# Optimization experiments

Hardware: AMD Instinct MI355X
Metric: run time of the kernel (lower is better)

The kernel has to match this reference:

```python
import jax, jax.numpy as jnp
import numpy as np


def setup_inputs() -> dict:
    key = jax.random.key(0)
    ks = jax.random.split(key, 8)
    B, S, D, H, E = 4, 2048, 1024, 2048, 8
    s = 0.02  # init scale
    return {
        "x": jax.random.normal(ks[0], (B, S, D), dtype=jnp.float32),
        "gate_w": jax.random.normal(ks[1], (E, D), dtype=jnp.float32) * s,
        "w1": jax.random.normal(ks[2], (E, H, D), dtype=jnp.float32) * s,
        "b1": jnp.zeros((E, H), dtype=jnp.float32),
        "w2": jax.random.normal(ks[3], (E, H, D), dtype=jnp.float32) * s,
        "b2": jnp.zeros((E, H), dtype=jnp.float32),
        "w3": jax.random.normal(ks[4], (E, D, H), dtype=jnp.float32) * s,
        "b3": jnp.zeros((E, D), dtype=jnp.float32),
        "topk": 2,
    }


def reference(x, gate_w, w1, b1, w2, b2, w3, b3, topk):
    D = x.shape[-1]
    E = gate_w.shape[0]
    xf = x.reshape(-1, D)                      # [T, D]
    T = xf.shape[0]

    logits = xf @ gate_w.T                     # [T, E]
    vals, idx = jax.lax.top_k(logits, topk)    # [T, K]
    wts = jax.nn.softmax(vals, axis=-1)        # [T, K]

    # per-token combine weight per expert (0 if expert not in top-k)
    comb = jnp.zeros((T, E), dtype=xf.dtype).at[
        jnp.arange(T)[:, None], idx
    ].add(wts)                                 # [T, E]

    out = jnp.zeros_like(xf)
    for e in range(E):  # fixed small loop over experts
        h = (xf @ w1[e].T + b1[e]) * jax.nn.silu(xf @ w2[e].T + b2[e])  # [T, H]
        y = h @ w3[e].T + b3[e]                                           # [T, D]
        out = out + comb[:, e:e + 1] * y
    return out.reshape(x.shape)
```

## Files before the change

### kernel.cpp

```cpp
#include <hip/hip_runtime.h>
#include <hip/hip_bf16.h>
#include <stdint.h>

#define T_TOK   8192
#define D_DIM   1024
#define H_DIM   2048
#define E_EXP   8
#define NP2     4096
#define BM      256
#define CAP     (2*T_TOK + E_EXP*BM)
#define MAXMB   (CAP/BM)

using f32x4 = __attribute__((ext_vector_type(4))) float;
using s16x4 = __attribute__((ext_vector_type(4))) short;
using s16x8 = __attribute__((ext_vector_type(8))) short;

__device__ __forceinline__ short bf16_of(float f) {
  union { float f; unsigned u; } v; v.f = f;
  unsigned r = v.u + 0x7FFFu + ((v.u >> 16) & 1u);
  return (short)(r >> 16);
}
__device__ __forceinline__ float f_of_bf16(short s) {
  union { unsigned u; float f; } v; v.u = ((unsigned)(unsigned short)s) << 16;
  return v.f;
}

__device__ __forceinline__ void gload16(const void* g, void* l) {
  __builtin_amdgcn_global_load_lds(
      (const __attribute__((address_space(1))) unsigned int*)g,
      (__attribute__((address_space(3))) unsigned int*)l, 16, 0, 0);
}

__global__ __launch_bounds__(256) void conv_w12(const float* __restrict__ w1,
                                                const float* __restrict__ w2,
                                                short* __restrict__ w12b) {
  int idx = blockIdx.x * 256 + threadIdx.x;
  int e = idx >> 20;
  int rem = idx & 0xFFFFF;
  int np = rem >> 8;
  int kc = rem & 255;
  int g = np >> 5, tt = np & 31, half = tt >> 4, srow = g * 16 + (tt & 15);
  const f32x4* src = (const f32x4*)(half ? w2 : w1) + ((size_t)e * H_DIM + srow) * 256 + kc;
  f32x4 v = *src;
  s16x4 o;
  o[0] = bf16_of(v[0]); o[1] = bf16_of(v[1]); o[2] = bf16_of(v[2]); o[3] = bf16_of(v[3]);
  ((s16x4*)w12b)[idx] = o;
}

__global__ __launch_bounds__(256) void conv_w3(const float* __restrict__ w3,
                                               short* __restrict__ w3b) {
  int idx = blockIdx.x * 256 + threadIdx.x;
  f32x4 v = ((const f32x4*)w3)[idx];
  s16x4 o;
  o[0] = bf16_of(v[0]); o[1] = bf16_of(v[1]); o[2] = bf16_of(v[2]); o[3] = bf16_of(v[3]);
  ((s16x4*)w3b)[idx] = o;
}

__global__ __launch_bounds__(256) void gate_kernel(const float* __restrict__ x,
                                                   const float* __restrict__ gw,
                                                   int* __restrict__ tok_e,
                                                   float* __restrict__ gatew) {
  __shared__ float g[E_EXP * D_DIM];
  int tid = threadIdx.x;
  for (int i = tid; i < E_EXP * 256; i += 256)
    ((f32x4*)g)[i] = ((const f32x4*)gw)[i];
  __syncthreads();
  int w = tid >> 6, lane = tid & 63;
  int t = blockIdx.x * 4 + w;
  float acc[E_EXP] = {};
  const f32x4* xrow = (const f32x4*)(x + (size_t)t * D_DIM);
#pragma unroll
  for (int i = 0; i < 4; ++i) {
    f32x4 xv = xrow[lane + 64 * i];
#pragma unroll
    for (int e = 0; e < E_EXP; ++e) {
      f32x4 gv = ((const f32x4*)g)[e * 256 + lane + 64 * i];
      acc[e] += xv[0] * gv[0] + xv[1] * gv[1] + xv[2] * gv[2] + xv[3] * gv[3];
    }
  }
#pragma unroll
  for (int e = 0; e < E_EXP; ++e)
#pragma unroll
    for (int off = 1; off < 64; off <<= 1)
      acc[e] += __shfl_xor(acc[e], off);
  if (lane == 0) {
    int i0 = 0; float v0 = acc[0];
    for (int e = 1; e < E_EXP; ++e) if (acc[e] > v0) { v0 = acc[e]; i0 = e; }
    int i1 = -1; float v1 = -1e30f;
    for (int e = 0; e < E_EXP; ++e) if (e != i0 && acc[e] > v1) { v1 = acc[e]; i1 = e; }
    float z = __expf(v1 - v0);
    tok_e[2 * t] = i0; tok_e[2 * t + 1] = i1;
    gatew[2 * t] = 1.f / (1.f + z); gatew[2 * t + 1] = z / (1.f + z);
  }
}

__global__ __launch_bounds__(256) void hist_kernel(const int* __restrict__ tok_e,
                                                   int* __restrict__ counts) {
  __shared__ int bc[E_EXP];
  const int tid = threadIdx.x, lane = tid & 63;
  if (tid < E_EXP) bc[tid] = 0;
  __syncthreads();
  const int4 v = ((const int4*)tok_e)[blockIdx.x * 256 + tid];
#pragma unroll
  for (int e = 0; e < E_EXP; ++e) {
    int cnt = __popcll(__ballot(v.x == e)) + __popcll(__ballot(v.y == e)) +
              __popcll(__ballot(v.z == e)) + __popcll(__ballot(v.w == e));
    if (lane == 0 && cnt) atomicAdd(&bc[e], cnt);
  }
  __syncthreads();
  if (tid < E_EXP && bc[tid]) atomicAdd(&counts[tid], bc[tid]);
}

__global__ void scan_kernel(const int* __restrict__ counts, int* __restrict__ off,
                            int* __restrict__ mb2e, int* __restrict__ mb2row) {
  if (threadIdx.x == 0 && blockIdx.x == 0) {
    int acc = 0, mb = 0;
    for (int e = 0; e < E_EXP; ++e) {
      off[e] = acc;
      int nb = (counts[e] + BM - 1) / BM;
      for (int b = 0; b < nb; ++b) { mb2e[mb] = e; mb2row[mb] = acc + b * BM; ++mb; }
      acc += nb * BM;
    }
    off[E_EXP] = acc;
    for (; mb < MAXMB; ++mb) mb2e[mb] = -1;
  }
}

__global__ __launch_bounds__(256) void assign_kernel(const int* __restrict__ tok_e,
                                                     const int* __restrict__ off,
                                                     int* __restrict__ fill,
                                                     int* __restrict__ perm,
                                                     int* __restrict__ tok_slot) {
  __shared__ int wcnt[4][E_EXP];
  __shared__ int wbase[4][E_EXP];
  const int tid = threadIdx.x, lane = tid & 63, wid = tid >> 6;
  if (tid < 32) wcnt[tid >> 3][tid & 7] = 0;
  __syncthreads();
  const int ent = blockIdx.x * 256 + tid;
  const int e = tok_e[ent];
  int myrank = 0;
#pragma unroll
  for (int e0 = 0; e0 < E_EXP; ++e0) {
    unsigned long long m = __ballot(e == e0);
    if (e == e0) {
      myrank = __popcll(m & ((1ull << lane) - 1ull));
      if (myrank == 0) wcnt[wid][e0] = __popcll(m);
    }
  }
  __syncthreads();
  if (tid < E_EXP) {
    int tot = wcnt[0][tid] + wcnt[1][tid] + wcnt[2][tid] + wcnt[3][tid];
    int base = tot ? atomicAdd(&fill[tid], tot) : 0;
#pragma unroll
    for (int w = 0; w < 4; ++w) { wbase[w][tid] = base; base += wcnt[w][tid]; }
  }
  __syncthreads();
  const int slot = off[e] + wbase[wid][e] + myrank;
  perm[slot] = ent >> 1;
  tok_slot[ent] = slot;
}

__global__ __launch_bounds__(128) void gather_kernel(const float* __restrict__ x,
                                                     const int* __restrict__ off,
                                                     const int* __restrict__ counts,
                                                     const int* __restrict__ perm,
                                                     short* __restrict__ Xp) {
  int s = blockIdx.x, tid = threadIdx.x;
  int e = -1;
#pragma unroll
  for (int i = 0; i < E_EXP; ++i)
    if (s >= off[i] && s < off[i + 1]) { e = i; break; }
  bool valid = false; int t = 0;
  if (e >= 0) { int r = s - off[e]; if (r < counts[e]) { valid = true; t = perm[s]; } }
  s16x8 o;
  if (valid) {
    const f32x4* xr = (const f32x4*)(x + (size_t)t * D_DIM);
    f32x4 a = xr[tid * 2], b = xr[tid * 2 + 1];
    o[0] = bf16_of(a[0]); o[1] = bf16_of(a[1]); o[2] = bf16_of(a[2]); o[3] = bf16_of(a[3]);
    o[4] = bf16_of(b[0]); o[5] = bf16_of(b[1]); o[6] = bf16_of(b[2]); o[7] = bf16_of(b[3]);
  } else {
#pragma unroll
    for (int j = 0; j < 8; ++j) o[j] = 0;
  }
  *(s16x8*)(Xp + (size_t)s * D_DIM + tid * 8) = o;
}

template <int K, int BN_, int EPI>
__global__ __launch_bounds__(512, (BN_ == 128) ? 4 : 2)
void gemm256(const short* __restrict__ A,
             const short* __restrict__ Bw,
             const int* __restrict__ mb2e,
             const int* __restrict__ mb2row,
             const float* __restrict__ biasA,
             const float* __restrict__ biasB,
             short* __restrict__ Out) {
  constexpr int NFULL = (EPI == 0) ? NP2 : D_DIM;
  constexpr int OUTLD = (EPI == 0) ? H_DIM : D_DIM;
  constexpr int KB = K * 2;
  constexpr int NT = K / 32;
  constexpr int NBF = BN_ / 64;
  constexpr int ABYTES = 16384;
  constexpr int BBYTES = BN_ * 64;
  constexpr int BUFB = ABYTES + BBYTES;
  constexpr int NB_LOADS = BN_ / 128;

  const int mb = blockIdx.y;
  const int e = mb2e[mb];
  if (e < 0) return;
  const int row0 = mb2row[mb];
  const int bn = blockIdx.x;

  __shared__ alignas(16) char lds[3 * BUFB];

  const int tid = threadIdx.x;
  const int lane = tid & 63;
  const int wid = tid >> 6;
  const int wr = wid >> 2;
  const int wc = wid & 3;

  const char* gA = (const char*)(A + (size_t)row0 * K);
  const char* gB = (const char*)(Bw + ((size_t)e * NFULL + (size_t)bn * BN_) * K);

  const int srow0 = tid >> 2, spq = tid & 3;

  f32x4 acc[8][NBF] = {};

  auto stageA = [&](int kt, int buf) {
#pragma unroll
    for (int r = 0; r < 2; ++r) {
      const int row = r * 128 + srow0;
      const int lq = spq ^ ((row >> 1) & 3);
      gload16(gA + (size_t)row * KB + kt * 64 + lq * 16,
              lds + buf * BUFB + r * 8192 + tid * 16);
    }
  };
  auto stageB = [&](int kt, int buf) {
#pragma unroll
    for (int r = 0; r < NB_LOADS; ++r) {
      const int row = r * 128 + srow0;
      const int lq = spq ^ ((row >> 1) & 3);
      gload16(gB + (size_t)row * KB + kt * 64 + lq * 16,
              lds + buf * BUFB + ABYTES + r * 8192 + tid * 16);
    }
  };

  stageA(0, 0); stageB(0, 0);
  stageA(1, 1); stageB(1, 1);
  if constexpr (BN_ == 256) asm volatile("s_waitcnt vmcnt(4)" ::: "memory");
  else                      asm volatile("s_waitcnt vmcnt(3)" ::: "memory");
  __builtin_amdgcn_s_barrier();
  __builtin_amdgcn_sched_barrier(0);

  const int qsw = (((lane >> 4) ^ ((lane >> 1) & 3)) << 4);
  const int arow = wr * 128 + (lane & 15);
  const int brow = wc * (BN_ / 4) + (lane & 15);

  int bc = 0;
  int b2 = 2;
  for (int t = 0; t < NT; ++t) {
    const char* bufb = lds + bc * BUFB;
    const char* pa = bufb + arow * 64 + qsw;
    const char* pb = bufb + ABYTES + brow * 64 + qsw;
    s16x8 av[4], bv[NBF];
#pragma unroll
    for (int f = 0; f < NBF; ++f) bv[f] = *(const s16x8*)(pb + f * 1024);
#pragma unroll
    for (int f = 0; f < 4; ++f) av[f] = *(const s16x8*)(pa + f * 1024);
    if (t + 2 < NT) stageA(t + 2, b2);
    __builtin_amdgcn_s_barrier();
    asm volatile("s_waitcnt lgkmcnt(0)" ::: "memory");
    __builtin_amdgcn_sched_barrier(0);
    __builtin_amdgcn_s_setprio(1);
#pragma unroll
    for (int mf = 0; mf < 4; ++mf)
#pragma unroll
      for (int nf = 0; nf < NBF; ++nf)
        acc[mf][nf] = __builtin_amdgcn_mfma_f32_16x16x32_bf16(av[mf], bv[nf], acc[mf][nf], 0, 0, 0);
    __builtin_amdgcn_s_setprio(0);
    __builtin_amdgcn_sched_barrier(0);
    __builtin_amdgcn_s_barrier();
#pragma unroll
    for (int f = 0; f < 4; ++f) av[f] = *(const s16x8*)(pa + (4 + f) * 1024);
    if (t + 2 < NT) stageB(t + 2, b2);
    __builtin_amdgcn_s_barrier();
    asm volatile("s_waitcnt lgkmcnt(0)" ::: "memory");
    __builtin_amdgcn_sched_barrier(0);
    __builtin_amdgcn_s_setprio(1);
#pragma unroll
    for (int mf = 0; mf < 4; ++mf)
#pragma unroll
      for (int nf = 0; nf < NBF; ++nf)
        acc[4 + mf][nf] = __builtin_amdgcn_mfma_f32_16x16x32_bf16(av[mf], bv[nf], acc[4 + mf][nf], 0, 0, 0);
    __builtin_amdgcn_s_setprio(0);
    __builtin_amdgcn_sched_barrier(0);
    if (t < NT - 1) {
      if (t == NT - 2)          asm volatile("s_waitcnt vmcnt(0)" ::: "memory");
      else if (BN_ == 256)      asm volatile("s_waitcnt vmcnt(4)" ::: "memory");
      else                      asm volatile("s_waitcnt vmcnt(3)" ::: "memory");
      __builtin_amdgcn_s_barrier();
      __builtin_amdgcn_sched_barrier(0);
    }
    bc = (bc == 2) ? 0 : bc + 1;
    b2 = (b2 == 2) ? 0 : b2 + 1;
  }

  if constexpr (EPI == 0) {
#pragma unroll
    for (int mf = 0; mf < 8; ++mf) {
      const int mrow = row0 + wr * 128 + mf * 16 + ((lane >> 4) << 2);
#pragma unroll
      for (int p = 0; p < 2; ++p) {
        const int hcol = bn * 128 + wc * 32 + p * 16 + (lane & 15);
        const float bb1 = biasA[e * H_DIM + hcol];
        const float bb2 = biasB[e * H_DIM + hcol];
        const f32x4 a1 = acc[mf][2 * p], a2 = acc[mf][2 * p + 1];
#pragma unroll
        for (int j = 0; j < 4; ++j) {
          float x1 = a1[j] + bb1, x2 = a2[j] + bb2;
          float hv = x1 * (x2 / (1.f + __expf(-x2)));
          Out[(size_t)(mrow + j) * OUTLD + hcol] = bf16_of(hv);
        }
      }
    }
  } else {
#pragma unroll
    for (int mf = 0; mf < 8; ++mf) {
      const int mrow = row0 + wr * 128 + mf * 16 + ((lane >> 4) << 2);
#pragma unroll
      for (int nf = 0; nf < NBF; ++nf) {
        const int col = bn * BN_ + wc * (BN_ / 4) + nf * 16 + (lane & 15);
        const float bb = biasA[e * D_DIM + col];
#pragma unroll
        for (int j = 0; j < 4; ++j)
          Out[(size_t)(mrow + j) * OUTLD + col] = bf16_of(acc[mf][nf][j] + bb);
      }
    }
  }
}

__global__ __launch_bounds__(128) void combine_kernel(const short* __restrict__ ysb,
                                                      const int* __restrict__ tok_slot,
                                                      const float* __restrict__ gatew,
                                                      float* __restrict__ out) {
  int t = blockIdx.x, tid = threadIdx.x;
  int s0 = tok_slot[2 * t], s1 = tok_slot[2 * t + 1];
  float w0 = gatew[2 * t], w1 = gatew[2 * t + 1];
  s16x8 a = *(const s16x8*)(ysb + (size_t)s0 * D_DIM + tid * 8);
  s16x8 b = *(const s16x8*)(ysb + (size_t)s1 * D_DIM + tid * 8);
  float* op = out + (size_t)t * D_DIM + tid * 8;
  f32x4 o0, o1;
#pragma unroll
  for (int j = 0; j < 4; ++j) o0[j] = w0 * f_of_bf16(a[j]) + w1 * f_of_bf16(b[j]);
#pragma unroll
  for (int j = 0; j < 4; ++j) o1[j] = w0 * f_of_bf16(a[4 + j]) + w1 * f_of_bf16(b[4 + j]);
  *(f32x4*)op = o0;
  *(f32x4*)(op + 4) = o1;
}

extern "C" void kernel_launch(void* const* d_in, const int* in_sizes, int n_in,
                              void* d_out, int out_size, void* d_ws, size_t ws_size,
                              hipStream_t stream) {
  const float* x  = (const float*)d_in[0];
  const float* gw = (const float*)d_in[1];
  const float* w1 = (const float*)d_in[2];
  const float* b1 = (const float*)d_in[3];
  const float* w2 = (const float*)d_in[4];
  const float* b2 = (const float*)d_in[5];
  const float* w3 = (const float*)d_in[6];
  const float* b3 = (const float*)d_in[7];
  float* out = (float*)d_out;

  char* ws = (char*)d_ws;
  size_t o = 0;
  short* w12b = (short*)(ws + o); o += (size_t)E_EXP * NP2 * D_DIM * 2;
  short* w3b  = (short*)(ws + o); o += (size_t)E_EXP * D_DIM * H_DIM * 2;
  short* Xp   = (short*)(ws + o); o += (size_t)CAP * D_DIM * 2;
  short* ysb  = Xp;
  short* hbuf = (short*)(ws + o); o += (size_t)CAP * H_DIM * 2;
  int* meta     = (int*)(ws + o);
  int* counts   = meta;
  int* fill     = meta + 8;
  int* offv     = meta + 16;
  int* mb2e     = meta + 32;
  int* mb2row   = meta + 112;
  int* tok_e    = meta + 192;
  int* tok_slot = tok_e + 2 * T_TOK;
  int* perm     = tok_slot + 2 * T_TOK;
  float* gatew  = (float*)(perm + CAP);
  const size_t ws_needed = o + (192 + 4 * T_TOK + CAP + 2 * T_TOK) * sizeof(int);
  if (ws_size < ws_needed) return;

  hipMemsetAsync(counts, 0, 16 * sizeof(int), stream);

  conv_w12<<<(E_EXP * NP2 * 256) / 256, 256, 0, stream>>>(w1, w2, w12b);
  conv_w3 <<<(E_EXP * D_DIM * (H_DIM / 4)) / 256, 256, 0, stream>>>(w3, w3b);
  gate_kernel<<<T_TOK / 4, 256, 0, stream>>>(x, gw, tok_e, gatew);
  hist_kernel<<<(2 * T_TOK) / 1024, 256, 0, stream>>>(tok_e, counts);
  scan_kernel<<<1, 64, 0, stream>>>(counts, offv, mb2e, mb2row);
  assign_kernel<<<(2 * T_TOK) / 256, 256, 0, stream>>>(tok_e, offv, fill, perm, tok_slot);
  gather_kernel<<<CAP, 128, 0, stream>>>(x, offv, counts, perm, Xp);
  gemm256<D_DIM, 256, 0><<<dim3(NP2 / 256, MAXMB), 512, 0, stream>>>(Xp, w12b, mb2e, mb2row, b1, b2, hbuf);
  gemm256<H_DIM, 128, 1><<<dim3(D_DIM / 128, MAXMB), 512, 0, stream>>>(hbuf, w3b, mb2e, mb2row, b3, b3, ysb);
  combine_kernel<<<T_TOK, 128, 0, stream>>>(ysb, tok_slot, gatew, out);
}
```

Before: 408.5 us.

## Add double-buffered K64 gate/up GEMM, trim barriers, widen down-proj tile

Replaces the first expert GEMM with a new kernel that stages 64-wide K slices into two 64KB LDS buffers and interleaves the next slice's global loads with four MFMA phases. In the generic GEMM it removes the intra-iteration barriers and lgkmcnt waits between the two MFMA halves. The down-projection is switched to a 256-wide N tile, which halves its grid columns. Dropping the barriers relies on the existing vmcnt/barrier at the end of each iteration to keep LDS reuse safe. The 128KB LDS kernel and the wider tile may lower occupancy.

```diff
diff --git a/kernel.cpp b/kernel.cpp
--- a/kernel.cpp
+++ b/kernel.cpp
@@ -183,6 +183,121 @@
     for (int j = 0; j < 8; ++j) o[j] = 0;
   }
   *(s16x8*)(Xp + (size_t)s * D_DIM + tid * 8) = o;
+}
+
+__global__ __launch_bounds__(512, 2)
+void gemm12_k64(const short* __restrict__ A,
+                const short* __restrict__ Bw,
+                const int* __restrict__ mb2e,
+                const int* __restrict__ mb2row,
+                const float* __restrict__ b1v,
+                const float* __restrict__ b2v,
+                short* __restrict__ Out) {
+  constexpr int K = D_DIM;
+  constexpr int NT = K / 64;
+  constexpr int BUFB = 65536;
+  __shared__ alignas(16) char lds[2 * BUFB];
+
+  const int mb = blockIdx.y;
+  const int e = mb2e[mb];
+  if (e < 0) return;
+  const int row0 = mb2row[mb];
+  const int bn = blockIdx.x;
+
+  const int tid = threadIdx.x;
+  const int lane = tid & 63;
+  const int wid = tid >> 6;
+  const int wr = wid >> 2, wc = wid & 3;
+
+  const char* gA = (const char*)(A + (size_t)row0 * K);
+  const char* gB = (const char*)(Bw + ((size_t)e * NP2 + (size_t)bn * 256) * K);
+
+  auto stage_unit = [&](const char* g, int kt, int ks, char* dst) {
+#pragma unroll
+    for (int r = 0; r < 2; ++r) {
+      const int row = r * 128 + (tid >> 2);
+      const int lq = (tid & 3) ^ ((row >> 1) & 3);
+      gload16(g + (size_t)row * (K * 2) + kt * 128 + ks * 64 + lq * 16,
+              dst + r * 8192 + tid * 16);
+    }
+  };
+
+  f32x4 acc[8][4] = {};
+
+  stage_unit(gB, 0, 0, lds + 32768);
+  stage_unit(gA, 0, 0, lds + 0);
+  stage_unit(gB, 0, 1, lds + 49152);
+  stage_unit(gA, 0, 1, lds + 16384);
+  asm volatile("s_waitcnt vmcnt(4)" ::: "memory");
+  __builtin_amdgcn_s_barrier();
+  __builtin_amdgcn_sched_barrier(0);
+
+  const int qsw = (((lane >> 4) ^ ((lane >> 1) & 3)) << 4);
+  const int arow = wr * 128 + (lane & 15);
+  const int brow = wc * 64 + (lane & 15);
+
+  for (int t = 0; t < NT; ++t) {
+    char* cur = lds + (t & 1) * BUFB;
+    char* nxt = lds + ((t + 1) & 1) * BUFB;
+    const bool more = (t + 1 < NT);
+    s16x8 bv[4];
+#pragma unroll
+    for (int p = 0; p < 4; ++p) {
+      const int ks = p >> 1, half = p & 1;
+      const char* abase = cur + ks * 16384;
+      s16x8 av[4];
+      if (half == 0) {
+        const char* bbase = cur + 32768 + ks * 16384;
+#pragma unroll
+        for (int f = 0; f < 4; ++f)
+          bv[f] = *(const s16x8*)(bbase + (size_t)(brow + f * 16) * 64 + qsw);
+      }
+#pragma unroll
+      for (int f = 0; f < 4; ++f)
+        av[f] = *(const s16x8*)(abase + (size_t)(arow + half * 64 + f * 16) * 64 + qsw);
+      if (more) {
+        if (p == 0)      stage_unit(gB, t + 1, 0, nxt + 32768);
+        else if (p == 1) stage_unit(gA, t + 1, 0, nxt + 0);
+        else if (p == 2) stage_unit(gB, t + 1, 1, nxt + 49152);
+        else             stage_unit(gA, t + 1, 1, nxt + 16384);
+      }
+      if (p == 1) {
+        if (t == NT - 1) asm volatile("s_waitcnt vmcnt(0)" ::: "memory");
+        else             asm volatile("s_waitcnt vmcnt(4)" ::: "memory");
+      }
+      if (p == 3 && t < NT - 1) asm volatile("s_waitcnt vmcnt(4)" ::: "memory");
+      __builtin_amdgcn_s_barrier();
+      asm volatile("s_waitcnt lgkmcnt(0)" ::: "memory");
+      __builtin_amdgcn_sched_barrier(0);
+      __builtin_amdgcn_s_setprio(1);
+#pragma unroll
+      for (int mf2 = 0; mf2 < 4; ++mf2)
+#pragma unroll
+        for (int nf = 0; nf < 4; ++nf)
+          acc[half * 4 + mf2][nf] =
+              __builtin_amdgcn_mfma_f32_16x16x32_bf16(av[mf2], bv[nf], acc[half * 4 + mf2][nf], 0, 0, 0);
+      __builtin_amdgcn_s_setprio(0);
+      __builtin_amdgcn_s_barrier();
+    }
+  }
+
+#pragma unroll
+  for (int mf = 0; mf < 8; ++mf) {
+    const int mrow = row0 + wr * 128 + (mf >> 2) * 64 + (mf & 3) * 16 + ((lane >> 4) << 2);
+#pragma unroll
+    for (int p = 0; p < 2; ++p) {
+      const int hcol = bn * 128 + wc * 32 + p * 16 + (lane & 15);
+      const float bb1 = b1v[e * H_DIM + hcol];
+      const float bb2 = b2v[e * H_DIM + hcol];
+      const f32x4 a1 = acc[mf][2 * p], a2 = acc[mf][2 * p + 1];
+#pragma unroll
+      for (int j = 0; j < 4; ++j) {
+        float x1 = a1[j] + bb1, x2 = a2[j] + bb2;
+        float hv = x1 * (x2 / (1.f + __expf(-x2)));
+        Out[(size_t)(mrow + j) * H_DIM + hcol] = bf16_of(hv);
+      }
+    }
+  }
 }
 
 template <int K, int BN_, int EPI>
@@ -267,9 +382,6 @@
 #pragma unroll
     for (int f = 0; f < 4; ++f) av[f] = *(const s16x8*)(pa + f * 1024);
     if (t + 2 < NT) stageA(t + 2, b2);
-    __builtin_amdgcn_s_barrier();
-    asm volatile("s_waitcnt lgkmcnt(0)" ::: "memory");
-    __builtin_amdgcn_sched_barrier(0);
     __builtin_amdgcn_s_setprio(1);
 #pragma unroll
     for (int mf = 0; mf < 4; ++mf)
@@ -277,14 +389,9 @@
       for (int nf = 0; nf < NBF; ++nf)
         acc[mf][nf] = __builtin_amdgcn_mfma_f32_16x16x32_bf16(av[mf], bv[nf], acc[mf][nf], 0, 0, 0);
     __builtin_amdgcn_s_setprio(0);
-    __builtin_amdgcn_sched_barrier(0);
-    __builtin_amdgcn_s_barrier();
 #pragma unroll
     for (int f = 0; f < 4; ++f) av[f] = *(const s16x8*)(pa + (4 + f) * 1024);
     if (t + 2 < NT) stageB(t + 2, b2);
-    __builtin_amdgcn_s_barrier();
-    asm volatile("s_waitcnt lgkmcnt(0)" ::: "memory");
-    __builtin_amdgcn_sched_barrier(0);
     __builtin_amdgcn_s_setprio(1);
 #pragma unroll
     for (int mf = 0; mf < 4; ++mf)
@@ -292,8 +399,9 @@
       for (int nf = 0; nf < NBF; ++nf)
         acc[4 + mf][nf] = __builtin_amdgcn_mfma_f32_16x16x32_bf16(av[mf], bv[nf], acc[4 + mf][nf], 0, 0, 0);
     __builtin_amdgcn_s_setprio(0);
-    __builtin_amdgcn_sched_barrier(0);
+
     if (t < NT - 1) {
+      __builtin_amdgcn_sched_barrier(0);
       if (t == NT - 2)          asm volatile("s_waitcnt vmcnt(0)" ::: "memory");
       else if (BN_ == 256)      asm volatile("s_waitcnt vmcnt(4)" ::: "memory");
       else                      asm volatile("s_waitcnt vmcnt(3)" ::: "memory");
@@ -399,7 +507,7 @@
   scan_kernel<<<1, 64, 0, stream>>>(counts, offv, mb2e, mb2row);
   assign_kernel<<<(2 * T_TOK) / 256, 256, 0, stream>>>(tok_e, offv, fill, perm, tok_slot);
   gather_kernel<<<CAP, 128, 0, stream>>>(x, offv, counts, perm, Xp);
-  gemm256<D_DIM, 256, 0><<<dim3(NP2 / 256, MAXMB), 512, 0, stream>>>(Xp, w12b, mb2e, mb2row, b1, b2, hbuf);
-  gemm256<H_DIM, 128, 1><<<dim3(D_DIM / 128, MAXMB), 512, 0, stream>>>(hbuf, w3b, mb2e, mb2row, b3, b3, ysb);
+  gemm12_k64<<<dim3(NP2 / 256, MAXMB), 512, 0, stream>>>(Xp, w12b, mb2e, mb2row, b1, b2, hbuf);
+  gemm256<H_DIM, 256, 1><<<dim3(D_DIM / 256, MAXMB), 512, 0, stream>>>(hbuf, w3b, mb2e, mb2row, b3, b3, ysb);
   combine_kernel<<<T_TOK, 128, 0, stream>>>(ysb, tok_slot, gatew, out);
 }
```

Measured after the change: 379.0 us. 7.2% less time.
